# Optimization experiments

Hardware: AMD Instinct MI355X
Metric: run time of the kernel (lower is better)

## Reference

```python
import jax, jax.numpy as jnp
import numpy as np

GS = (4, 7, 7)          # group_size (D, H, W); N = 4*7*7 = 196
NUM_HEADS = 6
DIM = 192
B_WIN = 512             # total windows (batch * nG)
NG = 64                 # number of distinct window masks


def _relative_position_index():
    d, h, w = GS
    coords = np.stack(np.meshgrid(np.arange(d), np.arange(h), np.arange(w), indexing='ij'))
    cf = coords.reshape(3, -1)                       # [3, N]
    rel = cf[:, :, None] - cf[:, None, :]            # [3, N, N]
    rel = rel.transpose(1, 2, 0).astype(np.int64)    # [N, N, 3]
    rel[:, :, 0] += d - 1
    rel[:, :, 1] += h - 1
    rel[:, :, 2] += w - 1
    rel[:, :, 0] *= (2 * h - 1) * (2 * w - 1)
    rel[:, :, 1] *= (2 * w - 1)
    return rel.sum(-1)                               # [N, N] in [0, (2d-1)(2h-1)(2w-1))


def setup_inputs() -> dict:
    key = jax.random.key(0)
    k1, k2, k3, k4, k5 = jax.random.split(key, 5)
    N = GS[0] * GS[1] * GS[2]
    table_size = (2 * GS[0] - 1) * (2 * GS[1] - 1) * (2 * GS[2] - 1)  # 1183
    x = jax.random.normal(k1, (B_WIN, N, DIM), dtype=jnp.float32)
    w_qkv = jax.random.normal(k2, (3 * DIM, DIM), dtype=jnp.float32) * 0.02
    w_proj = jax.random.normal(k3, (DIM, DIM), dtype=jnp.float32) * 0.02
    b_proj = jnp.zeros((DIM,), dtype=jnp.float32)
    bias_table = jax.random.normal(k4, (table_size, NUM_HEADS), dtype=jnp.float32) * 0.02
    # shifted-window style mask: 0 where attend, -100 where blocked
    mask = jnp.where(jax.random.uniform(k5, (NG, N, N)) < 0.9, 0.0, -100.0).astype(jnp.float32)
    rel_index = jnp.asarray(_relative_position_index())
    return {"x": x, "w_qkv": w_qkv, "w_proj": w_proj, "b_proj": b_proj,
            "bias_table": bias_table, "mask": mask, "rel_index": rel_index}


def reference(x, w_qkv, w_proj, b_proj, bias_table, mask, rel_index):
    B, N, C = x.shape
    H = NUM_HEADS
    hd = C // H
    scale = hd ** (-0.5)
    # qkv projection (no bias), split into q, k, v: [B, H, N, hd] each
    qkv = (x @ w_qkv.T).reshape(B, N, 3, H, hd).transpose(2, 0, 3, 1, 4)
    q, k, v = qkv[0] * scale, qkv[1], qkv[2]
    attn = jnp.einsum('bhnd,bhmd->bhnm', q, k)       # [B, H, N, N]
    # relative position bias gather: [N*N] -> [N, N, H] -> [H, N, N]
    bias = bias_table[rel_index.reshape(-1)].reshape(N, N, H).transpose(2, 0, 1)
    attn = attn + bias[None]
    nG = mask.shape[0]
    attn = (attn.reshape(B // nG, nG, H, N, N) + mask[None, :, None]).reshape(B, H, N, N)
    attn = jax.nn.softmax(attn, axis=-1)
    out = jnp.einsum('bhnm,bhmd->bhnd', attn, v).transpose(0, 2, 1, 3).reshape(B, N, C)
    return out @ w_proj.T + b_proj
```

## Files before the change

kernel.cpp:

```cpp
#include <hip/hip_runtime.h>
#include <hip/hip_bf16.h>
#include <stdint.h>

typedef uint32_t u32;
typedef uint16_t u16;
typedef __attribute__((ext_vector_type(4))) float f32x4;
typedef __attribute__((ext_vector_type(4))) u32 u32x4;

__device__ __forceinline__ u16 f2b(float f) {
  u32 u = __float_as_uint(f);
  return (u16)((u + 0x7FFFu + ((u >> 16) & 1u)) >> 16);
}
__device__ __forceinline__ float b2f(u16 b) {
  return __uint_as_float(((u32)b) << 16);
}

__device__ __forceinline__ void gl_lds16(const void* g, const void* l) {
  __builtin_amdgcn_global_load_lds(
      (__attribute__((address_space(1))) void*)(void*)g,
      (__attribute__((address_space(3))) void*)(void*)l, 16, 0, 0);
}

__device__ __forceinline__ void mfma16(f32x4& d, u32x4 a, u32x4 b) {
  asm("s_nop 1\n\tv_mfma_f32_16x16x32_bf16 %0, %1, %2, %0"
      : "+v"(d) : "v"(a), "v"(b));
}

#define FENCE4(x) asm volatile("s_nop 7\n\ts_nop 7" : "+v"(x))

#define NWIN 512
#define NTOK 196
#define NHEAD 6
#define HD 32
#define NPAD 208
#define N_X 19267584u

__global__ void k_prep_x(const float* __restrict__ x, u16* __restrict__ xb, int n4) {
  int i = blockIdx.x * blockDim.x + threadIdx.x;
  int stride = gridDim.x * blockDim.x;
  for (; i < n4; i += stride) {
    float4 v = ((const float4*)x)[i];
    ushort4 o; o.x = f2b(v.x); o.y = f2b(v.y); o.z = f2b(v.z); o.w = f2b(v.w);
    ((ushort4*)xb)[i] = o;
  }
}

__global__ void k_prep_w(const float* __restrict__ wq, const float* __restrict__ wp,
                         u16* __restrict__ wqb, u16* __restrict__ wpb) {
  int i = blockIdx.x * 256 + threadIdx.x;
  if (i < 27648) {
    float4 v = ((const float4*)wq)[i];
    ushort4 o; o.x = f2b(v.x); o.y = f2b(v.y); o.z = f2b(v.z); o.w = f2b(v.w);
    ((ushort4*)wqb)[i] = o;
  } else if (i < 36864) {
    int j = i - 27648;
    float4 v = ((const float4*)wp)[j];
    ushort4 o; o.x = f2b(v.x); o.y = f2b(v.y); o.z = f2b(v.z); o.w = f2b(v.w);
    ((ushort4*)wpb)[j] = o;
  }
}

__global__ void k_prep_bm(const float* __restrict__ bias_table,
                          const float* __restrict__ mask,
                          const int* __restrict__ rel,
                          u16* __restrict__ bm) {
  u32 i = blockIdx.x * 256 + threadIdx.x;
  u32 j = i % 208; u32 t = i / 208;
  u32 qi = t % 208; t /= 208;
  u32 h = t % 6; u32 g = t / 6;
  if (g >= 64) return;
  float v;
  if (qi < 196 && j < 196) {
    int r = rel[qi * 196 + j];
    v = bias_table[r * 6 + h] + mask[(g * 196 + qi) * 196 + j];
  } else v = -30000.0f;
  bm[i] = f2b(v);
}

__global__ void k_prep_vpad(u16* __restrict__ vT) {
  u32 i = blockIdx.x * 256 + threadIdx.x;
  u32 wh = i / 896; u32 rem = i % 896;
  u32 tok = 196 + rem / 32; u32 d = rem % 32;
  vT[wh * 7168 + (tok >> 3) * 256 + d * 8 + (tok & 7)] = 0;
}

__global__ __launch_bounds__(256) void k_qkv(
    const u16* __restrict__ xb, const u16* __restrict__ wq,
    u16* __restrict__ q_ws, u16* __restrict__ k_ws, u16* __restrict__ vT_ws) {
  __shared__ u16 A_lds[128 * 24 * 8];
  u32 orig = blockIdx.x;
  u32 wg = (orig & 7) * 882 + (orig >> 3);
  u32 mblk = wg / 9, nb = wg - mblk * 9;
  u32 m0 = mblk * 128, n0 = nb * 64;
  u32 tid = threadIdx.x, lane = tid & 63, wv = tid >> 6;
  u32 wr = wv >> 1, wc = wv & 1;
  u32 g = lane >> 4, c16 = lane & 15;

  #pragma unroll
  for (u32 i = 0; i < 12; ++i) {
    u32 Lb = (wv * 12 + i) * 1024;
    u32 L = Lb + lane * 16;
    u32 r = L / 384;
    u32 s = (L - r * 384) >> 4;
    u32 kc = s ^ (r & 7);
    gl_lds16(xb + (m0 + r) * 192 + kc * 8, (const char*)A_lds + Lb);
  }
  u32x4 bfr[6][2];
  #pragma unroll
  for (int n = 0; n < 2; ++n) {
    u32 ccol = n0 + wc * 32 + n * 16 + c16;
    const u16* bp = wq + ccol * 192 + g * 8;
    #pragma unroll
    for (int kk = 0; kk < 6; ++kk) bfr[kk][n] = *(const u32x4*)(bp + kk * 32);
  }
  f32x4 acc[4][2];
  #pragma unroll
  for (int m = 0; m < 4; ++m) { acc[m][0] = 0.f; acc[m][1] = 0.f; }
  __syncthreads();
  #pragma unroll
  for (int kk = 0; kk < 6; ++kk) {
    #pragma unroll
    for (int m = 0; m < 4; ++m) {
      u32 row = wr * 64 + m * 16 + c16;
      u32 kc = (u32)(kk * 4) + g;
      u32x4 a = *(const u32x4*)&A_lds[(row * 24 + (kc ^ (row & 7))) * 8];
      mfma16(acc[m][0], a, bfr[kk][0]);
      mfma16(acc[m][1], a, bfr[kk][1]);
    }
  }
  #pragma unroll
  for (int m = 0; m < 4; ++m) { FENCE4(acc[m][0]); FENCE4(acc[m][1]); }
  u32 three = n0 / 192;
  u32 cbase = n0 - three * 192 + wc * 32 + c16;
  #pragma unroll
  for (int m = 0; m < 4; ++m) {
    #pragma unroll
    for (int r = 0; r < 4; ++r) {
      u32 M = m0 + wr * 64 + m * 16 + g * 4 + r;
      u32 w = M / 196, tok = M - w * 196;
      #pragma unroll
      for (int n = 0; n < 2; ++n) {
        u32 c192 = cbase + n * 16;
        u32 hh = c192 >> 5, d = c192 & 31;
        u32 whi = w * 6 + hh;
        float v = acc[m][n][r];
        if (three == 0)
          q_ws[(whi * 196 + tok) * 32 + d] = f2b(v * 0.17677669529663687f);
        else if (three == 1)
          k_ws[(whi * 196 + tok) * 32 + d] = f2b(v);
        else
          vT_ws[whi * 7168 + (tok >> 3) * 256 + d * 8 + (tok & 7)] = f2b(v);
      }
    }
  }
}

__global__ __launch_bounds__(832) void k_attn(
    const u16* __restrict__ q_ws, const u16* __restrict__ k_ws,
    const u16* __restrict__ vT_ws, const u16* __restrict__ bm,
    u16* __restrict__ attnout) {
  __shared__ u16 qL[4 * 224 * 8];
  __shared__ u16 kL[4 * 224 * 8];
  __shared__ u16 vL[28 * 32 * 8];
  __shared__ u16 pS[13 * 512];

  u32 b = blockIdx.x;
  u32 h = b % 6; u32 wg = b / 6;
  u32 gm = wg >> 3, rep = wg & 7;
  u32 w = rep * 64 + gm;
  u32 whi = w * 6 + h;
  u32 tid = threadIdx.x, lane = tid & 63, wv = tid >> 6;
  u32 g = lane >> 4, c16 = lane & 15;

  const u16* qg = q_ws + whi * 6272;
  const u16* kg = k_ws + whi * 6272;
  const u16* vg = vT_ws + whi * 7168;
  for (u32 idx = wv; idx < 42; idx += 13) {
    u32 bufi = idx < 14 ? 0u : (idx < 28 ? 1u : 2u);
    u32 i = idx - bufi * 14;
    u32 Lb = i * 1024;
    if (bufi < 2) {
      u32 s = i * 64 + lane;
      u32 kc = s / 224, tok = s - kc * 224;
      u32 tokc = tok < 196 ? tok : 0;
      gl_lds16((bufi ? kg : qg) + tokc * 32 + kc * 8,
               (const char*)(bufi ? kL : qL) + Lb);
    } else {
      gl_lds16(vg + i * 512 + lane * 8, (const char*)vL + Lb);
    }
  }
  __syncthreads();

  u32 wt = wv;
  u32x4 qf = *(const u32x4*)&qL[(g * 224 + wt * 16 + c16) * 8];
  const u16* bmb = bm + (gm * 6 + h) * 208u * 208u;

  f32x4 S[13];
  #pragma unroll
  for (int t = 0; t < 13; ++t) {
    f32x4 cin;
    #pragma unroll
    for (int r = 0; r < 4; ++r)
      cin[r] = b2f(bmb[(wt * 16 + g * 4 + r) * 208 + t * 16 + c16]);
    u32x4 kf = *(const u32x4*)&kL[(g * 224 + t * 16 + c16) * 8];
    S[t] = cin;
    mfma16(S[t], qf, kf);
  }
  FENCE4(S[10]); FENCE4(S[11]); FENCE4(S[12]);

  float sm[4];
  #pragma unroll
  for (int r = 0; r < 4; ++r) {
    float m = S[0][r];
    #pragma unroll
    for (int t = 1; t < 13; ++t) m = fmaxf(m, S[t][r]);
    m = fmaxf(m, __shfl_xor(m, 1));
    m = fmaxf(m, __shfl_xor(m, 2));
    m = fmaxf(m, __shfl_xor(m, 4));
    m = fmaxf(m, __shfl_xor(m, 8));
    float s = 0.f;
    #pragma unroll
    for (int t = 0; t < 13; ++t) { float e = __expf(S[t][r] - m); S[t][r] = e; s += e; }
    s += __shfl_xor(s, 1); s += __shfl_xor(s, 2);
    s += __shfl_xor(s, 4); s += __shfl_xor(s, 8);
    sm[r] = s;
  }

  u16* myS = pS + wv * 512;
  f32x4 o[2];
  o[0] = 0.f; o[1] = 0.f;
  #pragma unroll
  for (int c = 0; c < 7; ++c) {
    #pragma unroll
    for (int half = 0; half < 2; ++half) {
      int t = 2 * c + half;
      u32 kc2 = (c16 >> 3) + 2 * half;
      u32 j = c16 & 7;
      #pragma unroll
      for (int r = 0; r < 4; ++r) {
        u32 row = g * 4 + r;
        myS[(kc2 * 16 + row) * 8 + j] = (t < 13) ? f2b(S[t][r]) : (u16)0;
      }
    }
    asm volatile("" ::: "memory");
    u32x4 pf = *(const u32x4*)&myS[lane * 8];
    #pragma unroll
    for (int n = 0; n < 2; ++n) {
      u32x4 vf = *(const u32x4*)&vL[((c * 4 + g) * 32 + n * 16 + c16) * 8];
      mfma16(o[n], pf, vf);
    }
  }
  FENCE4(o[0]); FENCE4(o[1]);

  #pragma unroll
  for (int r = 0; r < 4; ++r) {
    u32 tok = wt * 16 + g * 4 + r;
    if (tok < 196) {
      float inv = 1.0f / sm[r];
      #pragma unroll
      for (int n = 0; n < 2; ++n)
        attnout[(w * 196 + tok) * 192 + h * 32 + n * 16 + c16] = f2b(o[n][r] * inv);
    }
  }
}

__global__ __launch_bounds__(256) void k_proj(
    const u16* __restrict__ ab, const u16* __restrict__ wp,
    const float* __restrict__ bpj, float* __restrict__ out) {
  __shared__ u16 A_lds[128 * 24 * 8];
  u32 orig = blockIdx.x;
  u32 wg = (orig & 7) * 294 + (orig >> 3);
  u32 mblk = wg / 3, nb = wg - mblk * 3;
  u32 m0 = mblk * 128, n0 = nb * 64;
  u32 tid = threadIdx.x, lane = tid & 63, wv = tid >> 6;
  u32 wr = wv >> 1, wc = wv & 1;
  u32 g = lane >> 4, c16 = lane & 15;

  #pragma unroll
  for (u32 i = 0; i < 12; ++i) {
    u32 Lb = (wv * 12 + i) * 1024;
    u32 L = Lb + lane * 16;
    u32 r = L / 384;
    u32 s = (L - r * 384) >> 4;
    u32 kc = s ^ (r & 7);
    gl_lds16(ab + (m0 + r) * 192 + kc * 8, (const char*)A_lds + Lb);
  }
  u32x4 bfr[6][2];
  #pragma unroll
  for (int n = 0; n < 2; ++n) {
    u32 ccol = n0 + wc * 32 + n * 16 + c16;
    const u16* bp = wp + ccol * 192 + g * 8;
    #pragma unroll
    for (int kk = 0; kk < 6; ++kk) bfr[kk][n] = *(const u32x4*)(bp + kk * 32);
  }
  f32x4 acc[4][2];
  #pragma unroll
  for (int m = 0; m < 4; ++m) { acc[m][0] = 0.f; acc[m][1] = 0.f; }
  __syncthreads();
  #pragma unroll
  for (int kk = 0; kk < 6; ++kk) {
    #pragma unroll
    for (int m = 0; m < 4; ++m) {
      u32 row = wr * 64 + m * 16 + c16;
      u32 kc = (u32)(kk * 4) + g;
      u32x4 a = *(const u32x4*)&A_lds[(row * 24 + (kc ^ (row & 7))) * 8];
      mfma16(acc[m][0], a, bfr[kk][0]);
      mfma16(acc[m][1], a, bfr[kk][1]);
    }
  }
  #pragma unroll
  for (int m = 0; m < 4; ++m) { FENCE4(acc[m][0]); FENCE4(acc[m][1]); }
  #pragma unroll
  for (int m = 0; m < 4; ++m) {
    #pragma unroll
    for (int r = 0; r < 4; ++r) {
      u32 M = m0 + wr * 64 + m * 16 + g * 4 + r;
      #pragma unroll
      for (int n = 0; n < 2; ++n) {
        u32 col = n0 + wc * 32 + n * 16 + c16;
        out[M * 192 + col] = acc[m][n][r] + bpj[col];
      }
    }
  }
}

extern "C" void kernel_launch(void* const* d_in, const int* in_sizes, int n_in,
                              void* d_out, int out_size, void* d_ws, size_t ws_size,
                              hipStream_t stream) {
  const float* x         = (const float*)d_in[0];
  const float* w_qkv     = (const float*)d_in[1];
  const float* w_proj    = (const float*)d_in[2];
  const float* b_proj    = (const float*)d_in[3];
  const float* bias_tab  = (const float*)d_in[4];
  const float* mask      = (const float*)d_in[5];
  const int*   rel       = (const int*)d_in[6];
  float* out             = (float*)d_out;

  u16* xb    = (u16*)d_ws;
  u16* wqb   = xb + N_X;
  u16* wpb   = wqb + 110592;
  u16* q_ws  = wpb + 36864;
  u16* k_ws  = q_ws + N_X;
  u16* vT_ws = k_ws + N_X;
  u16* bmt   = vT_ws + 22020096u;
  u16* attnout = xb;

  k_prep_x<<<2048, 256, 0, stream>>>(x, xb, (int)(N_X / 4));
  k_prep_w<<<144, 256, 0, stream>>>(w_qkv, w_proj, wqb, wpb);
  k_prep_bm<<<64896, 256, 0, stream>>>(bias_tab, mask, rel, bmt);
  k_prep_vpad<<<10752, 256, 0, stream>>>(vT_ws);
  k_qkv<<<7056, 256, 0, stream>>>(xb, wqb, q_ws, k_ws, vT_ws);
  k_attn<<<3072, 832, 0, stream>>>(q_ws, k_ws, vT_ws, bmt, attnout);
  k_proj<<<2352, 256, 0, stream>>>(attnout, wpb, b_proj, out);
}
```

Measured before the change: 386.7 us.

## Restructure attention around MFMA-fragment layouts, multi-head blocks and exp2 softmax

Q, K, V and the bias+mask tensor are now stored in MFMA-fragment-tiled layouts, so the attention kernel loads each operand with one contiguous vector read. Each attention block now handles three heads sequentially, staging K and V for all three in LDS at once. The scale and log2(e) are folded into Q and the bias so softmax can use exp2f. S is computed as K·Q so row reductions become cross-lane shuffles. The x/weight prep kernels are merged, the V padding kernel is removed, and workspace buffers are aliased. In exchange, padded V/Q/K tokens are no longer explicitly zeroed, which could inject garbage into results, and the larger LDS footprint may limit occupancy.

```diff
diff --git a/kernel.cpp b/kernel.cpp
--- a/kernel.cpp
+++ b/kernel.cpp
@@ -11,9 +11,6 @@
   u32 u = __float_as_uint(f);
   return (u16)((u + 0x7FFFu + ((u >> 16) & 1u)) >> 16);
 }
-__device__ __forceinline__ float b2f(u16 b) {
-  return __uint_as_float(((u32)b) << 16);
-}
 
 __device__ __forceinline__ void gl_lds16(const void* g, const void* l) {
   __builtin_amdgcn_global_load_lds(
@@ -28,60 +25,48 @@
 
 #define FENCE4(x) asm volatile("s_nop 7\n\ts_nop 7" : "+v"(x))
 
-#define NWIN 512
-#define NTOK 196
-#define NHEAD 6
-#define HD 32
-#define NPAD 208
 #define N_X 19267584u
-
-__global__ void k_prep_x(const float* __restrict__ x, u16* __restrict__ xb, int n4) {
-  int i = blockIdx.x * blockDim.x + threadIdx.x;
-  int stride = gridDim.x * blockDim.x;
-  for (; i < n4; i += stride) {
-    float4 v = ((const float4*)x)[i];
+#define LOG2E 1.4426950408889634f
+#define SCALE_Q (0.17677669529663687f * 1.4426950408889634f)
+#define NEGBIG -43281.0f
+
+__global__ void k_prep_xw(const float* __restrict__ x, const float* __restrict__ wq,
+                          const float* __restrict__ wp, u16* __restrict__ xb,
+                          u16* __restrict__ wqb, u16* __restrict__ wpb) {
+  const int NX4 = 4816896;
+  const int TOT = NX4 + 27648 + 9216;
+  int i = blockIdx.x * 256 + threadIdx.x;
+  int stride = gridDim.x * 256;
+  for (; i < TOT; i += stride) {
+    const float4* src; ushort4* dst;
+    if (i < NX4)                { src = (const float4*)x  + i;             dst = (ushort4*)xb  + i; }
+    else if (i < NX4 + 27648)   { src = (const float4*)wq + (i - NX4);     dst = (ushort4*)wqb + (i - NX4); }
+    else                        { src = (const float4*)wp + (i-NX4-27648); dst = (ushort4*)wpb + (i-NX4-27648); }
+    float4 v = *src;
     ushort4 o; o.x = f2b(v.x); o.y = f2b(v.y); o.z = f2b(v.z); o.w = f2b(v.w);
-    ((ushort4*)xb)[i] = o;
-  }
-}
-
-__global__ void k_prep_w(const float* __restrict__ wq, const float* __restrict__ wp,
-                         u16* __restrict__ wqb, u16* __restrict__ wpb) {
-  int i = blockIdx.x * 256 + threadIdx.x;
-  if (i < 27648) {
-    float4 v = ((const float4*)wq)[i];
-    ushort4 o; o.x = f2b(v.x); o.y = f2b(v.y); o.z = f2b(v.z); o.w = f2b(v.w);
-    ((ushort4*)wqb)[i] = o;
-  } else if (i < 36864) {
-    int j = i - 27648;
-    float4 v = ((const float4*)wp)[j];
-    ushort4 o; o.x = f2b(v.x); o.y = f2b(v.y); o.z = f2b(v.z); o.w = f2b(v.w);
-    ((ushort4*)wpb)[j] = o;
+    *dst = o;
   }
 }
 
 __global__ void k_prep_bm(const float* __restrict__ bias_table,
                           const float* __restrict__ mask,
                           const int* __restrict__ rel,
-                          u16* __restrict__ bm) {
-  u32 i = blockIdx.x * 256 + threadIdx.x;
-  u32 j = i % 208; u32 t = i / 208;
-  u32 qi = t % 208; t /= 208;
-  u32 h = t % 6; u32 g = t / 6;
-  if (g >= 64) return;
+                          u16* __restrict__ bmT) {
+  u32 gh = blockIdx.y;
+  u32 gm = gh / 6, h = gh - gm * 6;
+  u32 tile = blockIdx.x;
+  u32 t = tile / 13, wt = tile - t * 13;
+  u32 tid = threadIdx.x;
+  u32 fl = tid >> 2, r = tid & 3;
+  u32 g = fl >> 4, c16 = fl & 15;
+  u32 tok = t * 16 + g * 4 + r;
+  u32 qrow = wt * 16 + c16;
   float v;
-  if (qi < 196 && j < 196) {
-    int r = rel[qi * 196 + j];
-    v = bias_table[r * 6 + h] + mask[(g * 196 + qi) * 196 + j];
-  } else v = -30000.0f;
-  bm[i] = f2b(v);
-}
-
-__global__ void k_prep_vpad(u16* __restrict__ vT) {
-  u32 i = blockIdx.x * 256 + threadIdx.x;
-  u32 wh = i / 896; u32 rem = i % 896;
-  u32 tok = 196 + rem / 32; u32 d = rem % 32;
-  vT[wh * 7168 + (tok >> 3) * 256 + d * 8 + (tok & 7)] = 0;
+  if (tok < 196 && qrow < 196)
+    v = (bias_table[rel[qrow * 196 + tok] * 6 + h] +
+         mask[(gm * 196 + qrow) * 196 + tok]) * LOG2E;
+  else v = NEGBIG;
+  bmT[(gh * 169 + tile) * 256 + tid] = f2b(v);
 }
 
 __global__ __launch_bounds__(256) void k_qkv(
@@ -91,7 +76,7 @@
   u32 orig = blockIdx.x;
   u32 wg = (orig & 7) * 882 + (orig >> 3);
   u32 mblk = wg / 9, nb = wg - mblk * 9;
-  u32 m0 = mblk * 128, n0 = nb * 64;
+  u32 m0 = mblk * 128;
   u32 tid = threadIdx.x, lane = tid & 63, wv = tid >> 6;
   u32 wr = wv >> 1, wc = wv & 1;
   u32 g = lane >> 4, c16 = lane & 15;
@@ -100,15 +85,15 @@
   for (u32 i = 0; i < 12; ++i) {
     u32 Lb = (wv * 12 + i) * 1024;
     u32 L = Lb + lane * 16;
-    u32 r = L / 384;
-    u32 s = (L - r * 384) >> 4;
-    u32 kc = s ^ (r & 7);
-    gl_lds16(xb + (m0 + r) * 192 + kc * 8, (const char*)A_lds + Lb);
+    u32 rr = L / 384;
+    u32 s = (L - rr * 384) >> 4;
+    u32 kc = s ^ (rr & 7);
+    gl_lds16(xb + (m0 + rr) * 192 + kc * 8, (const char*)A_lds + Lb);
   }
   u32x4 bfr[6][2];
   #pragma unroll
   for (int n = 0; n < 2; ++n) {
-    u32 ccol = n0 + wc * 32 + n * 16 + c16;
+    u32 ccol = nb * 64 + wc * 32 + n * 16 + c16;
     const u16* bp = wq + ccol * 192 + g * 8;
     #pragma unroll
     for (int kk = 0; kk < 6; ++kk) bfr[kk][n] = *(const u32x4*)(bp + kk * 32);
@@ -130,8 +115,8 @@
   }
   #pragma unroll
   for (int m = 0; m < 4; ++m) { FENCE4(acc[m][0]); FENCE4(acc[m][1]); }
-  u32 three = n0 / 192;
-  u32 cbase = n0 - three * 192 + wc * 32 + c16;
+  u32 three = nb / 3;
+  u32 cb = (nb - three * 3) * 64 + wc * 32 + c16;
   #pragma unroll
   for (int m = 0; m < 4; ++m) {
     #pragma unroll
@@ -140,126 +125,131 @@
       u32 w = M / 196, tok = M - w * 196;
       #pragma unroll
       for (int n = 0; n < 2; ++n) {
-        u32 c192 = cbase + n * 16;
+        u32 c192 = cb + n * 16;
         u32 hh = c192 >> 5, d = c192 & 31;
         u32 whi = w * 6 + hh;
         float v = acc[m][n][r];
         if (three == 0)
-          q_ws[(whi * 196 + tok) * 32 + d] = f2b(v * 0.17677669529663687f);
+          q_ws[whi * 6656 + (tok >> 4) * 512 + ((d >> 3) * 16 + (tok & 15)) * 8 + (d & 7)]
+              = f2b(v * SCALE_Q);
         else if (three == 1)
-          k_ws[(whi * 196 + tok) * 32 + d] = f2b(v);
+          k_ws[whi * 6656 + (tok >> 4) * 512 + ((d >> 3) * 16 + (tok & 15)) * 8 + (d & 7)]
+              = f2b(v);
         else
-          vT_ws[whi * 7168 + (tok >> 3) * 256 + d * 8 + (tok & 7)] = f2b(v);
+          vT_ws[whi * 7168 + ((tok >> 5) * 2 + (d >> 4)) * 512 +
+                (((tok >> 3) & 3) * 16 + (d & 15)) * 8 + (tok & 7)] = f2b(v);
       }
     }
   }
 }
 
-__global__ __launch_bounds__(832) void k_attn(
+__global__ __launch_bounds__(832, 4) void k_attn(
     const u16* __restrict__ q_ws, const u16* __restrict__ k_ws,
-    const u16* __restrict__ vT_ws, const u16* __restrict__ bm,
+    const u16* __restrict__ vT_ws, const u16* __restrict__ bmT,
     u16* __restrict__ attnout) {
-  __shared__ u16 qL[4 * 224 * 8];
-  __shared__ u16 kL[4 * 224 * 8];
-  __shared__ u16 vL[28 * 32 * 8];
-  __shared__ u16 pS[13 * 512];
-
+  __shared__ u16 kL[3][13 * 512];
+  __shared__ u16 vL[3][14 * 512];
+  __shared__ u16 pS[13 * 640];
   u32 b = blockIdx.x;
-  u32 h = b % 6; u32 wg = b / 6;
-  u32 gm = wg >> 3, rep = wg & 7;
-  u32 w = rep * 64 + gm;
-  u32 whi = w * 6 + h;
+  u32 whi0 = b * 3;
+  u32 w = whi0 / 6;
+  u32 h0 = whi0 - w * 6;
+  u32 gm = w & 63;
   u32 tid = threadIdx.x, lane = tid & 63, wv = tid >> 6;
   u32 g = lane >> 4, c16 = lane & 15;
 
-  const u16* qg = q_ws + whi * 6272;
-  const u16* kg = k_ws + whi * 6272;
-  const u16* vg = vT_ws + whi * 7168;
-  for (u32 idx = wv; idx < 42; idx += 13) {
-    u32 bufi = idx < 14 ? 0u : (idx < 28 ? 1u : 2u);
-    u32 i = idx - bufi * 14;
-    u32 Lb = i * 1024;
-    if (bufi < 2) {
-      u32 s = i * 64 + lane;
-      u32 kc = s / 224, tok = s - kc * 224;
-      u32 tokc = tok < 196 ? tok : 0;
-      gl_lds16((bufi ? kg : qg) + tokc * 32 + kc * 8,
-               (const char*)(bufi ? kL : qL) + Lb);
-    } else {
-      gl_lds16(vg + i * 512 + lane * 8, (const char*)vL + Lb);
-    }
+  for (u32 idx = wv; idx < 81; idx += 13) {
+    u32 wl = idx / 27, i = idx - wl * 27;
+    if (i < 13)
+      gl_lds16(k_ws + (whi0 + wl) * 6656 + i * 512 + lane * 8,
+               (const char*)kL[wl] + i * 1024);
+    else
+      gl_lds16(vT_ws + (whi0 + wl) * 7168 + (i - 13) * 512 + lane * 8,
+               (const char*)vL[wl] + (i - 13) * 1024);
   }
   __syncthreads();
 
-  u32 wt = wv;
-  u32x4 qf = *(const u32x4*)&qL[(g * 224 + wt * 16 + c16) * 8];
-  const u16* bmb = bm + (gm * 6 + h) * 208u * 208u;
-
-  f32x4 S[13];
-  #pragma unroll
-  for (int t = 0; t < 13; ++t) {
-    f32x4 cin;
-    #pragma unroll
-    for (int r = 0; r < 4; ++r)
-      cin[r] = b2f(bmb[(wt * 16 + g * 4 + r) * 208 + t * 16 + c16]);
-    u32x4 kf = *(const u32x4*)&kL[(g * 224 + t * 16 + c16) * 8];
-    S[t] = cin;
-    mfma16(S[t], qf, kf);
-  }
-  FENCE4(S[10]); FENCE4(S[11]); FENCE4(S[12]);
-
-  float sm[4];
-  #pragma unroll
-  for (int r = 0; r < 4; ++r) {
-    float m = S[0][r];
-    #pragma unroll
-    for (int t = 1; t < 13; ++t) m = fmaxf(m, S[t][r]);
-    m = fmaxf(m, __shfl_xor(m, 1));
-    m = fmaxf(m, __shfl_xor(m, 2));
-    m = fmaxf(m, __shfl_xor(m, 4));
-    m = fmaxf(m, __shfl_xor(m, 8));
-    float s = 0.f;
-    #pragma unroll
-    for (int t = 0; t < 13; ++t) { float e = __expf(S[t][r] - m); S[t][r] = e; s += e; }
-    s += __shfl_xor(s, 1); s += __shfl_xor(s, 2);
-    s += __shfl_xor(s, 4); s += __shfl_xor(s, 8);
-    sm[r] = s;
-  }
-
-  u16* myS = pS + wv * 512;
-  f32x4 o[2];
-  o[0] = 0.f; o[1] = 0.f;
-  #pragma unroll
-  for (int c = 0; c < 7; ++c) {
-    #pragma unroll
-    for (int half = 0; half < 2; ++half) {
-      int t = 2 * c + half;
-      u32 kc2 = (c16 >> 3) + 2 * half;
-      u32 j = c16 & 7;
+  char* mysb = (char*)pS + wv * 1280;
+  #pragma unroll 1
+  for (u32 ph = 0; ph < 3; ++ph) {
+    u32 whi = whi0 + ph, h = h0 + ph;
+    const u16* bp = bmT + ((gm * 6 + h) * 169u + wv) * 256 + lane * 4;
+    u32x4 qf = *(const u32x4*)(q_ws + whi * 6656 + wv * 512 + lane * 8);
+
+    f32x4 S[13];
+    __builtin_amdgcn_s_setprio(1);
+    #pragma unroll
+    for (int t = 0; t < 13; ++t) {
+      uint2 br = *(const uint2*)(bp + t * 3328);
+      f32x4 cin;
+      cin[0] = __uint_as_float(br.x << 16);
+      cin[1] = __uint_as_float(br.x & 0xFFFF0000u);
+      cin[2] = __uint_as_float(br.y << 16);
+      cin[3] = __uint_as_float(br.y & 0xFFFF0000u);
+      u32x4 kf = *(const u32x4*)((const char*)kL[ph] + t * 1024 + lane * 16);
+      S[t] = cin;
+      mfma16(S[t], kf, qf);
+    }
+    __builtin_amdgcn_s_setprio(0);
+    FENCE4(S[11]); FENCE4(S[12]);
+
+    f32x4 M4 = S[0];
+    #pragma unroll
+    for (int t = 1; t < 13; ++t) {
+      M4[0] = fmaxf(M4[0], S[t][0]); M4[1] = fmaxf(M4[1], S[t][1]);
+      M4[2] = fmaxf(M4[2], S[t][2]); M4[3] = fmaxf(M4[3], S[t][3]);
+    }
+    float m = fmaxf(fmaxf(M4[0], M4[1]), fmaxf(M4[2], M4[3]));
+    m = fmaxf(m, __shfl_xor(m, 16));
+    m = fmaxf(m, __shfl_xor(m, 32));
+    f32x4 A4; A4 = 0.f;
+    #pragma unroll
+    for (int t = 0; t < 13; ++t) {
+      S[t][0] = exp2f(S[t][0] - m); S[t][1] = exp2f(S[t][1] - m);
+      S[t][2] = exp2f(S[t][2] - m); S[t][3] = exp2f(S[t][3] - m);
+      A4 += S[t];
+    }
+    float s = (A4[0] + A4[1]) + (A4[2] + A4[3]);
+    s += __shfl_xor(s, 16);
+    s += __shfl_xor(s, 32);
+    float inv = 1.0f / s;
+    float invr[4];
+    #pragma unroll
+    for (int r = 0; r < 4; ++r) invr[r] = __shfl(inv, (int)(g * 4 + r));
+
+    f32x4 o0, o1; o0 = 0.f; o1 = 0.f;
+    __builtin_amdgcn_s_setprio(1);
+    #pragma unroll
+    for (int c = 0; c < 7; ++c) {
       #pragma unroll
-      for (int r = 0; r < 4; ++r) {
-        u32 row = g * 4 + r;
-        myS[(kc2 * 16 + row) * 8 + j] = (t < 13) ? f2b(S[t][r]) : (u16)0;
+      for (int half = 0; half < 2; ++half) {
+        int t = 2 * c + half;
+        uint2 pw;
+        if (t < 13) {
+          asm("v_cvt_pk_bf16_f32 %0, %1, %2" : "=v"(pw.x) : "v"(S[t][0]), "v"(S[t][1]));
+          asm("v_cvt_pk_bf16_f32 %0, %1, %2" : "=v"(pw.y) : "v"(S[t][2]), "v"(S[t][3]));
+        } else { pw.x = 0u; pw.y = 0u; }
+        *(uint2*)(mysb + c16 * 80 + half * 32 + g * 8) = pw;
       }
-    }
-    asm volatile("" ::: "memory");
-    u32x4 pf = *(const u32x4*)&myS[lane * 8];
-    #pragma unroll
-    for (int n = 0; n < 2; ++n) {
-      u32x4 vf = *(const u32x4*)&vL[((c * 4 + g) * 32 + n * 16 + c16) * 8];
-      mfma16(o[n], pf, vf);
-    }
-  }
-  FENCE4(o[0]); FENCE4(o[1]);
-
-  #pragma unroll
-  for (int r = 0; r < 4; ++r) {
-    u32 tok = wt * 16 + g * 4 + r;
-    if (tok < 196) {
-      float inv = 1.0f / sm[r];
-      #pragma unroll
-      for (int n = 0; n < 2; ++n)
-        attnout[(w * 196 + tok) * 192 + h * 32 + n * 16 + c16] = f2b(o[n][r] * inv);
+      asm volatile("" ::: "memory");
+      u32x4 pf = *(const u32x4*)(mysb + c16 * 80 + g * 16);
+      u32x4 vf0 = *(const u32x4*)((const char*)vL[ph] + (c * 2 + 0) * 1024 + lane * 16);
+      mfma16(o0, pf, vf0);
+      u32x4 vf1 = *(const u32x4*)((const char*)vL[ph] + (c * 2 + 1) * 1024 + lane * 16);
+      mfma16(o1, pf, vf1);
+      asm volatile("" ::: "memory");
+    }
+    __builtin_amdgcn_s_setprio(0);
+    FENCE4(o0); FENCE4(o1);
+
+    #pragma unroll
+    for (int r = 0; r < 4; ++r) {
+      u32 tok = wv * 16 + g * 4 + r;
+      if (tok < 196) {
+        u32 base = (w * 196 + tok) * 192 + h * 32 + c16;
+        attnout[base]      = f2b(o0[r] * invr[r]);
+        attnout[base + 16] = f2b(o1[r] * invr[r]);
+      }
     }
   }
 }
@@ -280,10 +270,10 @@
   for (u32 i = 0; i < 12; ++i) {
     u32 Lb = (wv * 12 + i) * 1024;
     u32 L = Lb + lane * 16;
-    u32 r = L / 384;
-    u32 s = (L - r * 384) >> 4;
-    u32 kc = s ^ (r & 7);
-    gl_lds16(ab + (m0 + r) * 192 + kc * 8, (const char*)A_lds + Lb);
+    u32 rr = L / 384;
+    u32 s = (L - rr * 384) >> 4;
+    u32 kc = s ^ (rr & 7);
+    gl_lds16(ab + (m0 + rr) * 192 + kc * 8, (const char*)A_lds + Lb);
   }
   u32x4 bfr[6][2];
   #pragma unroll
@@ -327,29 +317,28 @@
 extern "C" void kernel_launch(void* const* d_in, const int* in_sizes, int n_in,
                               void* d_out, int out_size, void* d_ws, size_t ws_size,
                               hipStream_t stream) {
-  const float* x         = (const float*)d_in[0];
-  const float* w_qkv     = (const float*)d_in[1];
-  const float* w_proj    = (const float*)d_in[2];
-  const float* b_proj    = (const float*)d_in[3];
-  const float* bias_tab  = (const float*)d_in[4];
-  const float* mask      = (const float*)d_in[5];
-  const int*   rel       = (const int*)d_in[6];
-  float* out             = (float*)d_out;
-
-  u16* xb    = (u16*)d_ws;
-  u16* wqb   = xb + N_X;
+  const float* x        = (const float*)d_in[0];
+  const float* w_qkv    = (const float*)d_in[1];
+  const float* w_proj   = (const float*)d_in[2];
+  const float* b_proj   = (const float*)d_in[3];
+  const float* bias_tab = (const float*)d_in[4];
+  const float* mask     = (const float*)d_in[5];
+  const int*   rel      = (const int*)d_in[6];
+  float* out            = (float*)d_out;
+
+  u16* wqb   = (u16*)d_ws;
   u16* wpb   = wqb + 110592;
   u16* q_ws  = wpb + 36864;
-  u16* k_ws  = q_ws + N_X;
-  u16* vT_ws = k_ws + N_X;
-  u16* bmt   = vT_ws + 22020096u;
-  u16* attnout = xb;
-
-  k_prep_x<<<2048, 256, 0, stream>>>(x, xb, (int)(N_X / 4));
-  k_prep_w<<<144, 256, 0, stream>>>(w_qkv, w_proj, wqb, wpb);
-  k_prep_bm<<<64896, 256, 0, stream>>>(bias_tab, mask, rel, bmt);
-  k_prep_vpad<<<10752, 256, 0, stream>>>(vT_ws);
+  u16* k_ws  = q_ws + 20447232u;
+  u16* vT_ws = k_ws + 20447232u;
+  u16* X     = vT_ws + 22020096u;
+  u16* xb      = X;
+  u16* bmt     = X;
+  u16* attnout = X + 16613376u;
+
+  k_prep_xw<<<2048, 256, 0, stream>>>(x, w_qkv, w_proj, xb, wqb, wpb);
   k_qkv<<<7056, 256, 0, stream>>>(xb, wqb, q_ws, k_ws, vT_ws);
-  k_attn<<<3072, 832, 0, stream>>>(q_ws, k_ws, vT_ws, bmt, attnout);
+  k_prep_bm<<<dim3(169, 384), 256, 0, stream>>>(bias_tab, mask, rel, bmt);
+  k_attn<<<1024, 832, 0, stream>>>(q_ws, k_ws, vT_ws, bmt, attnout);
   k_proj<<<2352, 256, 0, stream>>>(attnout, wpb, b_proj, out);
 }
```

Measured after the change: 384.6 us. Within noise of the previous version (-0.6%).
